# Kernel tuning notes

Hardware: AMD Instinct MI355X
Metric: run time of the kernel (lower is better)

## Reference

```python
import jax, jax.numpy as jnp
import numpy as np

N_NODES = 50000
N_EDGES = 800000
HEADS = 4
IN_CH = 128
HID_CH = 32   # per-head, conv1
OUT_CH = 32   # per-head, conv2
N_GRAPHS = 64
NEG_SLOPE = 0.2
BN_EPS = 1e-5


def gat_conv(x, src, dst, n_nodes, W, att_src, att_dst, bias):
    """PyG-style GATConv (concat heads). x:[N,Fin], W:[Fin,H*C], att_*:[H,C], bias:[H*C]."""
    H, C = att_src.shape
    h = (x @ W).reshape(n_nodes, H, C)                      # [N,H,C]
    a_src = jnp.einsum('nhc,hc->nh', h, att_src)            # [N,H]
    a_dst = jnp.einsum('nhc,hc->nh', h, att_dst)            # [N,H]
    e = jax.nn.leaky_relu(a_src[src] + a_dst[dst], NEG_SLOPE)  # [E,H]
    # segment softmax over incoming edges of each destination node
    e_max = jax.ops.segment_max(e, dst, num_segments=n_nodes)  # [N,H]
    alpha = jnp.exp(e - e_max[dst])                         # [E,H]
    denom = jax.ops.segment_sum(alpha, dst, num_segments=n_nodes)  # [N,H]
    alpha = alpha / denom[dst]
    msg = alpha[:, :, None] * h[src]                        # [E,H,C]
    out = jax.ops.segment_sum(msg, dst, num_segments=n_nodes)  # [N,H,C]
    return out.reshape(n_nodes, H * C) + bias


def setup_inputs() -> dict:
    key = jax.random.key(0)
    ks = jax.random.split(key, 12)
    d1 = HID_CH * HEADS  # 128
    d2 = OUT_CH * HEADS  # 128
    s_in = 1.0 / np.sqrt(IN_CH)
    s_h = 1.0 / np.sqrt(d1)
    return {
        'x': jax.random.normal(ks[0], (N_NODES, IN_CH), jnp.float32),
        'edge_index': jax.random.randint(ks[1], (2, N_EDGES), 0, N_NODES, jnp.int32),
        'batch': jnp.sort(jax.random.randint(ks[2], (N_NODES,), 0, N_GRAPHS, jnp.int32)),
        'W1': jax.random.normal(ks[3], (IN_CH, d1), jnp.float32) * s_in,
        'att_src1': jax.random.normal(ks[4], (HEADS, HID_CH), jnp.float32) * s_h,
        'att_dst1': jax.random.normal(ks[5], (HEADS, HID_CH), jnp.float32) * s_h,
        'bias1': jnp.zeros((d1,), jnp.float32),
        'gamma1': jnp.ones((d1,), jnp.float32),
        'beta1': jnp.zeros((d1,), jnp.float32),
        'W2': jax.random.normal(ks[6], (d1, d2), jnp.float32) * s_h,
        'att_src2': jax.random.normal(ks[7], (HEADS, OUT_CH), jnp.float32) * s_h,
        'att_dst2': jax.random.normal(ks[8], (HEADS, OUT_CH), jnp.float32) * s_h,
        'bias2': jnp.zeros((d2,), jnp.float32),
    }


def reference(x, edge_index, batch, W1, att_src1, att_dst1, bias1,
              gamma1, beta1, W2, att_src2, att_dst2, bias2):
    n = x.shape[0]
    loops = jnp.arange(n, dtype=edge_index.dtype)
    src = jnp.concatenate([edge_index[0], loops])  # add self-loops (PyG default)
    dst = jnp.concatenate([edge_index[1], loops])

    h = gat_conv(x, src, dst, n, W1, att_src1, att_dst1, bias1)
    # BatchNorm1d (batch statistics, biased variance), then ELU; dropout is inference no-op
    mu = h.mean(axis=0)
    var = h.var(axis=0)
    h = (h - mu) * jax.lax.rsqrt(var + BN_EPS) * gamma1 + beta1
    h = jax.nn.elu(h)

    h2 = gat_conv(h, src, dst, n, W2, att_src2, att_dst2, bias2)  # [N, OUT_CH*HEADS]

    # global mean pool over graphs
    ones = jnp.ones((n,), h2.dtype)
    counts = jax.ops.segment_sum(ones, batch, num_segments=N_GRAPHS)
    pooled = jax.ops.segment_sum(h2, batch, num_segments=N_GRAPHS)
    graph_rep = pooled / jnp.maximum(counts, 1.0)[:, None]
    return (h2, graph_rep)
```

## Files before the change

### kernel.cpp

```cpp
#include <hip/hip_runtime.h>

#define NN 50000
#define NE 800000
#define ET 850000
#define NG 64
#define D  128
#define NB 196
#define CAP 5120
#define CHUNK 8192

typedef unsigned short u16;
typedef unsigned int   u32;
typedef short bf16x8 __attribute__((ext_vector_type(8)));
typedef float f32x4  __attribute__((ext_vector_type(4)));

__device__ __forceinline__ u16 f2b(float f){
  u32 u = __float_as_uint(f);
  u32 r = (u + 0x7fffu + ((u >> 16) & 1u)) >> 16;
  return (u16)r;
}
__device__ __forceinline__ u32 pack2(float a, float b){
  return (u32)f2b(a) | ((u32)f2b(b) << 16);
}
__device__ __forceinline__ float lo16f(u32 u){ return __uint_as_float(u << 16); }
__device__ __forceinline__ float hi16f(u32 u){ return __uint_as_float(u & 0xffff0000u); }

__global__ void k_init(int* gCur, float* bsum, float* bsq, float* pooled){
  int i = blockIdx.x*256 + threadIdx.x;
  if (i < 256) gCur[i] = 0;
  if (i < 128){ bsum[i] = 0.f; bsq[i] = 0.f; }
  if (i < NG*D) pooled[i] = 0.f;
}

__global__ __launch_bounds__(256) void k_bucket(const int* __restrict__ srcE, const int* __restrict__ dstE,
                                                int* __restrict__ gCur, int* __restrict__ temp){
  __shared__ int hist[256], hbase[256], hpos[256], gbase[256];
  __shared__ int sorted[CHUNK];
  int tid = threadIdx.x;
  int e0 = blockIdx.x * CHUNK;
  int e1 = e0 + CHUNK; if (e1 > NE) e1 = NE;
  int cnt = e1 - e0;
  hist[tid] = 0;
  __syncthreads();
  for (int i = e0 + tid; i < e1; i += 256)
    atomicAdd(&hist[(u32)dstE[i] >> 8], 1);
  __syncthreads();
  int v = hist[tid];
  hbase[tid] = v;
  __syncthreads();
  for (int off = 1; off < 256; off <<= 1){
    int t = (tid >= off) ? hbase[tid-off] : 0;
    __syncthreads();
    hbase[tid] += t;
    __syncthreads();
  }
  int excl = hbase[tid] - v;
  __syncthreads();
  hbase[tid] = excl;
  hpos[tid]  = excl;
  __syncthreads();
  for (int i = e0 + tid; i < e1; i += 256){
    int d = dstE[i], sr = srcE[i];
    int idx = atomicAdd(&hpos[(u32)d >> 8], 1);
    sorted[idx] = (d << 16) | sr;
  }
  __syncthreads();
  if (tid < NB && hist[tid] > 0)
    gbase[tid] = atomicAdd(&gCur[tid], hist[tid]);
  __syncthreads();
  for (int i = tid; i < cnt; i += 256){
    int vv = sorted[i];
    int b = (u32)vv >> 24;
    int pos = gbase[b] + (i - hbase[b]);
    if (pos < CAP) temp[b*CAP + pos] = vv;
  }
}

__global__ void k_bstart(const int* __restrict__ gCur, int* __restrict__ bstart, int* __restrict__ offs){
  __shared__ int s[256];
  int tid = threadIdx.x;
  int nodes = (tid < NB) ? ((tid == NB-1) ? (NN - (NB-1)*256) : 256) : 0;
  int v = (tid < NB) ? gCur[tid] + nodes : 0;
  s[tid] = v;
  __syncthreads();
  for (int off = 1; off < 256; off <<= 1){
    int t = (tid >= off) ? s[tid-off] : 0;
    __syncthreads();
    s[tid] += t;
    __syncthreads();
  }
  if (tid < NB) bstart[tid] = s[tid] - v;
  if (tid == 0) offs[NN] = ET;
}

__global__ __launch_bounds__(256) void k_place(const int* __restrict__ temp, const int* __restrict__ gCur,
                                               const int* __restrict__ bstart, int* __restrict__ offs,
                                               int* __restrict__ srcs){
  __shared__ int cnt256[256], pfx[256], pos[256];
  int b = blockIdx.x, tid = threadIdx.x;
  int n0 = b << 8;
  int nNodes = NN - n0; if (nNodes > 256) nNodes = 256;
  int count = gCur[b];
  const int* tb = temp + b*CAP;
  cnt256[tid] = 0;
  __syncthreads();
  for (int i = tid; i < count; i += 256)
    atomicAdd(&cnt256[((u32)tb[i] >> 16) & 255], 1);
  __syncthreads();
  int own = cnt256[tid] + (tid < nNodes ? 1 : 0);
  pfx[tid] = own;
  __syncthreads();
  for (int off = 1; off < 256; off <<= 1){
    int t = (tid >= off) ? pfx[tid-off] : 0;
    __syncthreads();
    pfx[tid] += t;
    __syncthreads();
  }
  int excl = pfx[tid] - own;
  __syncthreads();
  pos[tid] = excl + 1;
  __syncthreads();
  int base = bstart[b];
  if (tid < nNodes){
    offs[n0 + tid] = base + excl;
    srcs[base + excl] = n0 + tid;
  }
  for (int i = tid; i < count; i += 256){
    int vv = tb[i];
    int d = ((u32)vv >> 16) & 255;
    int k = atomicAdd(&pos[d], 1);
    srcs[base + k] = vv & 0xFFFF;
  }
}

template<int FUSE_BN>
__global__ __launch_bounds__(512) void k_gemm(const float* __restrict__ X, const float* __restrict__ W,
                                              u16* __restrict__ Ybf,
                                              const float* __restrict__ att_s, const float* __restrict__ att_d,
                                              float* __restrict__ asrc, float* __restrict__ adst,
                                              const float* __restrict__ bsc, const float* __restrict__ bsh,
                                              int nrows){
  __shared__ u16 Xs[128*132];
  __shared__ u16 WT[128*132];
  int tid = threadIdx.x;
  int row0 = blockIdx.x * 128;
  #pragma unroll
  for (int t = 0; t < 8; t++){
    int i = tid + t*512;
    int r = i >> 5, k4 = i & 31;
    int gr = row0 + r;
    float4 v = (gr < nrows) ? ((const float4*)(X + (size_t)gr*D))[k4]
                            : make_float4(0.f,0.f,0.f,0.f);
    if (FUSE_BN){
      float4 sc = ((const float4*)bsc)[k4];
      float4 sh = ((const float4*)bsh)[k4];
      v.x = fmaf(v.x, sc.x, sh.x); v.y = fmaf(v.y, sc.y, sh.y);
      v.z = fmaf(v.z, sc.z, sh.z); v.w = fmaf(v.w, sc.w, sh.w);
      v.x = v.x > 0.f ? v.x : expm1f(v.x);
      v.y = v.y > 0.f ? v.y : expm1f(v.y);
      v.z = v.z > 0.f ? v.z : expm1f(v.z);
      v.w = v.w > 0.f ? v.w : expm1f(v.w);
    }
    *(uint2*)&Xs[r*132 + k4*4] = make_uint2(pack2(v.x, v.y), pack2(v.z, v.w));
  }
  {
    int c = tid & 127, kp = tid >> 7;
    #pragma unroll
    for (int t = 0; t < 16; t++){
      int kk = kp + t*4;
      float w0 = W[(size_t)(2*kk)*D + c];
      float w1 = W[(size_t)(2*kk+1)*D + c];
      *(u32*)&WT[c*132 + 2*kk] = pack2(w0, w1);
    }
  }
  __syncthreads();
  int w = tid >> 6, l = tid & 63;
  int l15 = l & 15, lq = l >> 4;
  int cw = w*16;
  bf16x8 bfr[4];
  #pragma unroll
  for (int ks = 0; ks < 4; ks++)
    bfr[ks] = *(const bf16x8*)&WT[(cw + l15)*132 + ks*32 + lq*8];
  f32x4 acc[8];
  #pragma unroll
  for (int m = 0; m < 8; m++) acc[m] = (f32x4){0.f,0.f,0.f,0.f};
  #pragma unroll
  for (int m = 0; m < 8; m++){
    #pragma unroll
    for (int ks = 0; ks < 4; ks++){
      bf16x8 af = *(const bf16x8*)&Xs[(m*16 + l15)*132 + ks*32 + lq*8];
      acc[m] = __builtin_amdgcn_mfma_f32_16x16x32_bf16(af, bfr[ks], acc[m], 0, 0, 0);
    }
  }
  __syncthreads();
  float* sDotS = (float*)Xs;
  float* sDotD = sDotS + 1024;
  {
    float as_c = att_s[cw + l15];
    float ad_c = att_d[cw + l15];
    #pragma unroll
    for (int m = 0; m < 8; m++){
      #pragma unroll
      for (int i = 0; i < 4; i++){
        float ps = acc[m][i] * as_c;
        float pd = acc[m][i] * ad_c;
        #pragma unroll
        for (int msk = 1; msk <= 8; msk <<= 1){
          ps += __shfl_xor(ps, msk);
          pd += __shfl_xor(pd, msk);
        }
        if (l15 == 0){
          int r = m*16 + lq*4 + i;
          sDotS[w*128 + r] = ps;
          sDotD[w*128 + r] = pd;
        }
      }
    }
  }
  #pragma unroll
  for (int m = 0; m < 8; m++){
    #pragma unroll
    for (int i = 0; i < 4; i++){
      float v = acc[m][i];
      float nb = __shfl_xor(v, 1);
      if (!(l & 1)){
        int gr = row0 + m*16 + lq*4 + i;
        if (gr < nrows)
          *(u32*)&Ybf[(size_t)gr*D + cw + l15] = pack2(v, nb);
      }
    }
  }
  __syncthreads();
  {
    int r = tid >> 2, h = tid & 3;
    int gr = row0 + r;
    if (gr < nrows){
      asrc[gr*4 + h] = sDotS[(2*h)*128 + r] + sDotS[(2*h+1)*128 + r];
      adst[gr*4 + h] = sDotD[(2*h)*128 + r] + sDotD[(2*h+1)*128 + r];
    }
  }
}

__global__ __launch_bounds__(256) void k_edge(
                       const u16* __restrict__ hb, const float* __restrict__ asrc,
                       const float* __restrict__ adst, const int* __restrict__ offs,
                       const int* __restrict__ srcs, const float* __restrict__ bias,
                       float* __restrict__ out){
  __shared__ uint2 sPk[4][4][17];
  int w = threadIdx.x >> 6;
  int lane = threadIdx.x & 63;
  int n = blockIdx.x*4 + w;
  int off0 = offs[n];
  int deg  = offs[n+1] - off0;
  int hd = lane >> 4, j16 = lane & 15;
  float adh = adst[n*4 + hd];
  int half = lane >> 5, q = lane & 31;
  int hg = q >> 3;
  int qb = q*8;
  float denp = 0.f;
  float acc0=0.f, acc1=0.f, acc2=0.f, acc3=0.f;
  const char* hbase = (const char*)hb;
  const int* sp = srcs + off0;
  int sj = (j16 < deg) ? sp[j16] : 0;
  float av = asrc[sj*4 + hd];
  for (int base = 0; base < deg; base += 16){
    int lim = deg - base; if (lim > 16) lim = 16;
    int nbase = base + 16;
    bool hasn = (nbase < deg);
    int sjn = 0;
    if (hasn){
      int idx = nbase + j16;
      sjn = (idx < deg) ? sp[idx] : 0;
    }
    float al;
    if (j16 < lim){
      float e = av + adh;
      e = e > 0.f ? e : 0.2f*e;
      al = __expf(e);
    } else al = 0.f;
    denp += al;
    sPk[w][hd][j16] = make_uint2((u32)sj << 8, __float_as_uint(al));
    float avn = hasn ? asrc[sjn*4 + hd] : 0.f;
    if (lim == 16){
      uint2 p0 = sPk[w][hg][half],      p1 = sPk[w][hg][2+half];
      uint2 p2 = sPk[w][hg][4+half],    p3 = sPk[w][hg][6+half];
      uint2 p4 = sPk[w][hg][8+half],    p5 = sPk[w][hg][10+half];
      uint2 p6 = sPk[w][hg][12+half],   p7 = sPk[w][hg][14+half];
      uint2 v0 = *(const uint2*)(hbase + p0.x + qb);
      uint2 v1 = *(const uint2*)(hbase + p1.x + qb);
      uint2 v2 = *(const uint2*)(hbase + p2.x + qb);
      uint2 v3 = *(const uint2*)(hbase + p3.x + qb);
      uint2 v4 = *(const uint2*)(hbase + p4.x + qb);
      uint2 v5 = *(const uint2*)(hbase + p5.x + qb);
      uint2 v6 = *(const uint2*)(hbase + p6.x + qb);
      uint2 v7 = *(const uint2*)(hbase + p7.x + qb);
      float a0 = __uint_as_float(p0.y), a1 = __uint_as_float(p1.y);
      float a2 = __uint_as_float(p2.y), a3 = __uint_as_float(p3.y);
      float a4 = __uint_as_float(p4.y), a5 = __uint_as_float(p5.y);
      float a6 = __uint_as_float(p6.y), a7 = __uint_as_float(p7.y);
      acc0 = fmaf(a0, lo16f(v0.x), acc0); acc1 = fmaf(a0, hi16f(v0.x), acc1);
      acc2 = fmaf(a0, lo16f(v0.y), acc2); acc3 = fmaf(a0, hi16f(v0.y), acc3);
      acc0 = fmaf(a1, lo16f(v1.x), acc0); acc1 = fmaf(a1, hi16f(v1.x), acc1);
      acc2 = fmaf(a1, lo16f(v1.y), acc2); acc3 = fmaf(a1, hi16f(v1.y), acc3);
      acc0 = fmaf(a2, lo16f(v2.x), acc0); acc1 = fmaf(a2, hi16f(v2.x), acc1);
      acc2 = fmaf(a2, lo16f(v2.y), acc2); acc3 = fmaf(a2, hi16f(v2.y), acc3);
      acc0 = fmaf(a3, lo16f(v3.x), acc0); acc1 = fmaf(a3, hi16f(v3.x), acc1);
      acc2 = fmaf(a3, lo16f(v3.y), acc2); acc3 = fmaf(a3, hi16f(v3.y), acc3);
      acc0 = fmaf(a4, lo16f(v4.x), acc0); acc1 = fmaf(a4, hi16f(v4.x), acc1);
      acc2 = fmaf(a4, lo16f(v4.y), acc2); acc3 = fmaf(a4, hi16f(v4.y), acc3);
      acc0 = fmaf(a5, lo16f(v5.x), acc0); acc1 = fmaf(a5, hi16f(v5.x), acc1);
      acc2 = fmaf(a5, lo16f(v5.y), acc2); acc3 = fmaf(a5, hi16f(v5.y), acc3);
      acc0 = fmaf(a6, lo16f(v6.x), acc0); acc1 = fmaf(a6, hi16f(v6.x), acc1);
      acc2 = fmaf(a6, lo16f(v6.y), acc2); acc3 = fmaf(a6, hi16f(v6.y), acc3);
      acc0 = fmaf(a7, lo16f(v7.x), acc0); acc1 = fmaf(a7, hi16f(v7.x), acc1);
      acc2 = fmaf(a7, lo16f(v7.y), acc2); acc3 = fmaf(a7, hi16f(v7.y), acc3);
    } else {
      for (int j = 0; j < lim; j += 8){
        uint2 pA = sPk[w][hg][j+half],   pB = sPk[w][hg][j+2+half];
        uint2 pC = sPk[w][hg][j+4+half], pD = sPk[w][hg][j+6+half];
        uint2 vA = *(const uint2*)(hbase + pA.x + qb);
        uint2 vB = *(const uint2*)(hbase + pB.x + qb);
        uint2 vC = *(const uint2*)(hbase + pC.x + qb);
        uint2 vD = *(const uint2*)(hbase + pD.x + qb);
        float aA = __uint_as_float(pA.y), aB = __uint_as_float(pB.y);
        float aC = __uint_as_float(pC.y), aD = __uint_as_float(pD.y);
        acc0 = fmaf(aA, lo16f(vA.x), acc0); acc1 = fmaf(aA, hi16f(vA.x), acc1);
        acc2 = fmaf(aA, lo16f(vA.y), acc2); acc3 = fmaf(aA, hi16f(vA.y), acc3);
        acc0 = fmaf(aB, lo16f(vB.x), acc0); acc1 = fmaf(aB, hi16f(vB.x), acc1);
        acc2 = fmaf(aB, lo16f(vB.y), acc2); acc3 = fmaf(aB, hi16f(vB.y), acc3);
        acc0 = fmaf(aC, lo16f(vC.x), acc0); acc1 = fmaf(aC, hi16f(vC.x), acc1);
        acc2 = fmaf(aC, lo16f(vC.y), acc2); acc3 = fmaf(aC, hi16f(vC.y), acc3);
        acc0 = fmaf(aD, lo16f(vD.x), acc0); acc1 = fmaf(aD, hi16f(vD.x), acc1);
        acc2 = fmaf(aD, lo16f(vD.y), acc2); acc3 = fmaf(aD, hi16f(vD.y), acc3);
      }
    }
    sj = sjn; av = avn;
  }
  denp += __shfl_xor(denp, 1);
  denp += __shfl_xor(denp, 2);
  denp += __shfl_xor(denp, 4);
  denp += __shfl_xor(denp, 8);
  acc0 += __shfl_xor(acc0, 32);
  acc1 += __shfl_xor(acc1, 32);
  acc2 += __shfl_xor(acc2, 32);
  acc3 += __shfl_xor(acc3, 32);
  float inv = 1.f / __shfl(denp, hg*16);
  if (half == 0){
    int cb = q*4;
    float4 o;
    o.x = acc0*inv + bias[cb];
    o.y = acc1*inv + bias[cb+1];
    o.z = acc2*inv + bias[cb+2];
    o.w = acc3*inv + bias[cb+3];
    ((float4*)(out + (size_t)n*D))[q] = o;
  }
}

__global__ __launch_bounds__(256) void k_bnstat(const float* __restrict__ B,
                                                float* __restrict__ bsum, float* __restrict__ bsq){
  __shared__ float sS[256], sQ[256];
  int tid = threadIdx.x;
  int c = tid & 127;
  int rr = tid >> 7;
  int r0 = blockIdx.x * 64;
  int r1 = r0 + 64; if (r1 > NN) r1 = NN;
  float s = 0.f, qv = 0.f;
  for (int r = r0 + rr; r < r1; r += 2){
    float v = B[(size_t)r*D + c];
    s += v; qv += v*v;
  }
  sS[tid] = s; sQ[tid] = qv;
  __syncthreads();
  if (tid < 128){
    atomicAdd(&bsum[c], sS[tid] + sS[tid+128]);
    atomicAdd(&bsq[c],  sQ[tid] + sQ[tid+128]);
  }
}

__global__ void k_bnfin(const float* __restrict__ bsum, const float* __restrict__ bsq,
                        const float* __restrict__ gamma, const float* __restrict__ beta,
                        float* __restrict__ scale, float* __restrict__ shift){
  int c = threadIdx.x;
  float mu  = bsum[c] * (1.f/NN);
  float var = bsq[c] * (1.f/NN) - mu*mu;
  float sc  = gamma[c] * rsqrtf(var + 1e-5f);
  scale[c] = sc;
  shift[c] = beta[c] - mu*sc;
}

#define POOL_ROWS 50
__global__ void k_poolA(const float* __restrict__ h2, const int* __restrict__ batch,
                        float* __restrict__ pooled){
  int c = threadIdx.x & 127;
  int half = threadIdx.x >> 7;
  int r0 = blockIdx.x * POOL_ROWS;
  int r1 = r0 + POOL_ROWS; if (r1 > NN) r1 = NN;
  float s = 0.f; int g = -1;
  for (int r = r0 + half; r < r1; r += 2){
    int bg = batch[r];
    if (bg != g){
      if (g >= 0) atomicAdd(&pooled[g*D + c], s);
      g = bg; s = 0.f;
    }
    s += h2[(size_t)r*D + c];
  }
  if (g >= 0) atomicAdd(&pooled[g*D + c], s);
}

__global__ void k_poolB(const float* __restrict__ pooled, const int* __restrict__ batch,
                        float* __restrict__ out){
  int g = blockIdx.x;
  int c = threadIdx.x;
  int lo = 0, hi = NN;
  while (lo < hi){ int mid = (lo+hi) >> 1; if (batch[mid] < g) lo = mid+1; else hi = mid; }
  int a = lo, b = NN;
  while (a < b){ int mid = (a+b) >> 1; if (batch[mid] < g+1) a = mid+1; else b = mid; }
  int cntg = a - lo;
  out[g*D + c] = pooled[g*D + c] / (float)(cntg > 1 ? cntg : 1);
}

extern "C" void kernel_launch(void* const* d_in, const int* in_sizes, int n_in,
                              void* d_out, int out_size, void* d_ws, size_t ws_size,
                              hipStream_t stream){
  (void)in_sizes; (void)n_in; (void)out_size; (void)ws_size;
  const float* x   = (const float*)d_in[0];
  const int* ei    = (const int*)d_in[1];
  const int* batch = (const int*)d_in[2];
  const float* W1  = (const float*)d_in[3];
  const float* as1 = (const float*)d_in[4];
  const float* ad1 = (const float*)d_in[5];
  const float* b1  = (const float*)d_in[6];
  const float* g1  = (const float*)d_in[7];
  const float* be1 = (const float*)d_in[8];
  const float* W2  = (const float*)d_in[9];
  const float* as2 = (const float*)d_in[10];
  const float* ad2 = (const float*)d_in[11];
  const float* b2  = (const float*)d_in[12];
  float* outp = (float*)d_out;

  float* B    = (float*)d_ws;
  float* asr  = B + 6400000;
  float* ads  = asr + 200000;
  float* bsum = ads + 200000;
  float* bsq  = bsum + 128;
  float* bsc  = bsq + 128;
  float* bsh  = bsc + 128;
  float* pooled = bsh + 128;
  int* gCur   = (int*)(pooled + NG*D);
  int* bstart = gCur + 256;
  int* offs   = bstart + 256;
  int* srcs   = offs + (NN+1);
  int* temp   = srcs + ET;
  u16* hb     = (u16*)(temp + NB*CAP);

  const int* srcE = ei;
  const int* dstE = ei + NE;

  k_init<<<32, 256, 0, stream>>>(gCur, bsum, bsq, pooled);
  k_gemm<0><<<391, 512, 0, stream>>>(x, W1, hb, as1, ad1, asr, ads, nullptr, nullptr, NN);
  k_bucket<<<(NE + CHUNK - 1)/CHUNK, 256, 0, stream>>>(srcE, dstE, gCur, temp);
  k_bstart<<<1, 256, 0, stream>>>(gCur, bstart, offs);
  k_place<<<NB, 256, 0, stream>>>(temp, gCur, bstart, offs, srcs);
  k_edge<<<NN/4, 256, 0, stream>>>(hb, asr, ads, offs, srcs, b1, B);
  k_bnstat<<<782, 256, 0, stream>>>(B, bsum, bsq);
  k_bnfin<<<1, 128, 0, stream>>>(bsum, bsq, g1, be1, bsc, bsh);
  k_gemm<1><<<391, 512, 0, stream>>>(B, W2, hb, as2, ad2, asr, ads, bsc, bsh, NN);
  k_edge<<<NN/4, 256, 0, stream>>>(hb, asr, ads, offs, srcs, b2, outp);
  k_poolA<<<(NN + POOL_ROWS - 1)/POOL_ROWS, 256, 0, stream>>>(outp, batch, pooled);
  k_poolB<<<NG, 128, 0, stream>>>(pooled, batch, outp + 6400000);
}
```

Measured before the change: 233.9 us.

## Use head-major feature layout and one-head-per-block edge aggregation

Node features and source attention scores are now stored head-major, so each block in the edge kernel handles one head for four nodes. That gives 4x more blocks, and each gather is a contiguous 64-byte head slice processed 8 edges at a time per wave. The weight matrices are transposed and converted to bf16 once by a new prep kernel, so every GEMM block no longer re-transposes W. The LDS row pitch is also changed to 136. The risk is that offsets, srcs and adst are read four times, each gather is smaller, and there are two extra launches.

```diff
diff --git a/kernel.cpp b/kernel.cpp
--- a/kernel.cpp
+++ b/kernel.cpp
@@ -30,6 +30,13 @@
   if (i < 256) gCur[i] = 0;
   if (i < 128){ bsum[i] = 0.f; bsq[i] = 0.f; }
   if (i < NG*D) pooled[i] = 0.f;
+}
+
+__global__ void k_prepw(const float* __restrict__ W, u16* __restrict__ WTb){
+  for (int i = blockIdx.x*256 + threadIdx.x; i < D*D; i += gridDim.x*256){
+    int c = i >> 7, k = i & 127;
+    WTb[i] = f2b(W[(size_t)k*D + c]);
+  }
 }
 
 __global__ __launch_bounds__(256) void k_bucket(const int* __restrict__ srcE, const int* __restrict__ dstE,
@@ -134,14 +141,14 @@
 }
 
 template<int FUSE_BN>
-__global__ __launch_bounds__(512) void k_gemm(const float* __restrict__ X, const float* __restrict__ W,
-                                              u16* __restrict__ Ybf,
+__global__ __launch_bounds__(512) void k_gemm(const float* __restrict__ X, const u16* __restrict__ WTb,
+                                              u16* __restrict__ hbT,
                                               const float* __restrict__ att_s, const float* __restrict__ att_d,
-                                              float* __restrict__ asrc, float* __restrict__ adst,
+                                              float* __restrict__ asrcT, float* __restrict__ adst,
                                               const float* __restrict__ bsc, const float* __restrict__ bsh,
                                               int nrows){
-  __shared__ u16 Xs[128*132];
-  __shared__ u16 WT[128*132];
+  __shared__ u16 Xs[128*136];
+  __shared__ u16 WT[128*136];
   int tid = threadIdx.x;
   int row0 = blockIdx.x * 128;
   #pragma unroll
@@ -161,17 +168,14 @@
       v.z = v.z > 0.f ? v.z : expm1f(v.z);
       v.w = v.w > 0.f ? v.w : expm1f(v.w);
     }
-    *(uint2*)&Xs[r*132 + k4*4] = make_uint2(pack2(v.x, v.y), pack2(v.z, v.w));
-  }
-  {
-    int c = tid & 127, kp = tid >> 7;
-    #pragma unroll
-    for (int t = 0; t < 16; t++){
-      int kk = kp + t*4;
-      float w0 = W[(size_t)(2*kk)*D + c];
-      float w1 = W[(size_t)(2*kk+1)*D + c];
-      *(u32*)&WT[c*132 + 2*kk] = pack2(w0, w1);
-    }
+    *(uint2*)&Xs[r*136 + k4*4] = make_uint2(pack2(v.x, v.y), pack2(v.z, v.w));
+  }
+  #pragma unroll
+  for (int t = 0; t < 4; t++){
+    int i = tid + t*512;
+    int c = i >> 4, k16 = i & 15;
+    uint4 vv = ((const uint4*)WTb)[i];
+    *(uint4*)&WT[c*136 + k16*8] = vv;
   }
   __syncthreads();
   int w = tid >> 6, l = tid & 63;
@@ -180,7 +184,7 @@
   bf16x8 bfr[4];
   #pragma unroll
   for (int ks = 0; ks < 4; ks++)
-    bfr[ks] = *(const bf16x8*)&WT[(cw + l15)*132 + ks*32 + lq*8];
+    bfr[ks] = *(const bf16x8*)&WT[(cw + l15)*136 + ks*32 + lq*8];
   f32x4 acc[8];
   #pragma unroll
   for (int m = 0; m < 8; m++) acc[m] = (f32x4){0.f,0.f,0.f,0.f};
@@ -188,7 +192,7 @@
   for (int m = 0; m < 8; m++){
     #pragma unroll
     for (int ks = 0; ks < 4; ks++){
-      bf16x8 af = *(const bf16x8*)&Xs[(m*16 + l15)*132 + ks*32 + lq*8];
+      bf16x8 af = *(const bf16x8*)&Xs[(m*16 + l15)*136 + ks*32 + lq*8];
       acc[m] = __builtin_amdgcn_mfma_f32_16x16x32_bf16(af, bfr[ks], acc[m], 0, 0, 0);
     }
   }
@@ -225,8 +229,11 @@
       float nb = __shfl_xor(v, 1);
       if (!(l & 1)){
         int gr = row0 + m*16 + lq*4 + i;
-        if (gr < nrows)
-          *(u32*)&Ybf[(size_t)gr*D + cw + l15] = pack2(v, nb);
+        if (gr < nrows){
+          int col = cw + l15;
+          int head = col >> 5, c32 = col & 31;
+          *(u32*)&hbT[((size_t)head*NN + gr)*32 + c32] = pack2(v, nb);
+        }
       }
     }
   }
@@ -235,124 +242,82 @@
     int r = tid >> 2, h = tid & 3;
     int gr = row0 + r;
     if (gr < nrows){
-      asrc[gr*4 + h] = sDotS[(2*h)*128 + r] + sDotS[(2*h+1)*128 + r];
+      asrcT[(size_t)h*NN + gr] = sDotS[(2*h)*128 + r] + sDotS[(2*h+1)*128 + r];
       adst[gr*4 + h] = sDotD[(2*h)*128 + r] + sDotD[(2*h+1)*128 + r];
     }
   }
 }
 
 __global__ __launch_bounds__(256) void k_edge(
-                       const u16* __restrict__ hb, const float* __restrict__ asrc,
+                       const u16* __restrict__ hbT, const float* __restrict__ asrcT,
                        const float* __restrict__ adst, const int* __restrict__ offs,
                        const int* __restrict__ srcs, const float* __restrict__ bias,
                        float* __restrict__ out){
-  __shared__ uint2 sPk[4][4][17];
+  __shared__ uint2 sAl[4][64];
   int w = threadIdx.x >> 6;
   int lane = threadIdx.x & 63;
-  int n = blockIdx.x*4 + w;
+  int h = blockIdx.x & 3;
+  int n = (blockIdx.x >> 2)*4 + w;
   int off0 = offs[n];
   int deg  = offs[n+1] - off0;
-  int hd = lane >> 4, j16 = lane & 15;
-  float adh = adst[n*4 + hd];
-  int half = lane >> 5, q = lane & 31;
-  int hg = q >> 3;
-  int qb = q*8;
+  float adh = adst[n*4 + h];
+  const float* asp = asrcT + (size_t)h*NN;
+  const char* hbase = (const char*)(hbT + (size_t)h*NN*32);
+  const int* sp = srcs + off0;
+  int g8 = lane & 7;
+  int eg = lane >> 3;
   float denp = 0.f;
   float acc0=0.f, acc1=0.f, acc2=0.f, acc3=0.f;
-  const char* hbase = (const char*)hb;
-  const int* sp = srcs + off0;
-  int sj = (j16 < deg) ? sp[j16] : 0;
-  float av = asrc[sj*4 + hd];
-  for (int base = 0; base < deg; base += 16){
-    int lim = deg - base; if (lim > 16) lim = 16;
-    int nbase = base + 16;
-    bool hasn = (nbase < deg);
-    int sjn = 0;
-    if (hasn){
-      int idx = nbase + j16;
-      sjn = (idx < deg) ? sp[idx] : 0;
-    }
-    float al;
-    if (j16 < lim){
-      float e = av + adh;
+  for (int base = 0; base < deg; base += 64){
+    int lim = deg - base; if (lim > 64) lim = 64;
+    int sj = 0; float al = 0.f;
+    if (lane < lim){
+      sj = sp[base + lane];
+      float e = asp[sj] + adh;
       e = e > 0.f ? e : 0.2f*e;
       al = __expf(e);
-    } else al = 0.f;
+    }
     denp += al;
-    sPk[w][hd][j16] = make_uint2((u32)sj << 8, __float_as_uint(al));
-    float avn = hasn ? asrc[sjn*4 + hd] : 0.f;
-    if (lim == 16){
-      uint2 p0 = sPk[w][hg][half],      p1 = sPk[w][hg][2+half];
-      uint2 p2 = sPk[w][hg][4+half],    p3 = sPk[w][hg][6+half];
-      uint2 p4 = sPk[w][hg][8+half],    p5 = sPk[w][hg][10+half];
-      uint2 p6 = sPk[w][hg][12+half],   p7 = sPk[w][hg][14+half];
-      uint2 v0 = *(const uint2*)(hbase + p0.x + qb);
-      uint2 v1 = *(const uint2*)(hbase + p1.x + qb);
-      uint2 v2 = *(const uint2*)(hbase + p2.x + qb);
-      uint2 v3 = *(const uint2*)(hbase + p3.x + qb);
-      uint2 v4 = *(const uint2*)(hbase + p4.x + qb);
-      uint2 v5 = *(const uint2*)(hbase + p5.x + qb);
-      uint2 v6 = *(const uint2*)(hbase + p6.x + qb);
-      uint2 v7 = *(const uint2*)(hbase + p7.x + qb);
-      float a0 = __uint_as_float(p0.y), a1 = __uint_as_float(p1.y);
-      float a2 = __uint_as_float(p2.y), a3 = __uint_as_float(p3.y);
-      float a4 = __uint_as_float(p4.y), a5 = __uint_as_float(p5.y);
-      float a6 = __uint_as_float(p6.y), a7 = __uint_as_float(p7.y);
-      acc0 = fmaf(a0, lo16f(v0.x), acc0); acc1 = fmaf(a0, hi16f(v0.x), acc1);
-      acc2 = fmaf(a0, lo16f(v0.y), acc2); acc3 = fmaf(a0, hi16f(v0.y), acc3);
-      acc0 = fmaf(a1, lo16f(v1.x), acc0); acc1 = fmaf(a1, hi16f(v1.x), acc1);
-      acc2 = fmaf(a1, lo16f(v1.y), acc2); acc3 = fmaf(a1, hi16f(v1.y), acc3);
-      acc0 = fmaf(a2, lo16f(v2.x), acc0); acc1 = fmaf(a2, hi16f(v2.x), acc1);
-      acc2 = fmaf(a2, lo16f(v2.y), acc2); acc3 = fmaf(a2, hi16f(v2.y), acc3);
-      acc0 = fmaf(a3, lo16f(v3.x), acc0); acc1 = fmaf(a3, hi16f(v3.x), acc1);
-      acc2 = fmaf(a3, lo16f(v3.y), acc2); acc3 = fmaf(a3, hi16f(v3.y), acc3);
-      acc0 = fmaf(a4, lo16f(v4.x), acc0); acc1 = fmaf(a4, hi16f(v4.x), acc1);
-      acc2 = fmaf(a4, lo16f(v4.y), acc2); acc3 = fmaf(a4, hi16f(v4.y), acc3);
-      acc0 = fmaf(a5, lo16f(v5.x), acc0); acc1 = fmaf(a5, hi16f(v5.x), acc1);
-      acc2 = fmaf(a5, lo16f(v5.y), acc2); acc3 = fmaf(a5, hi16f(v5.y), acc3);
-      acc0 = fmaf(a6, lo16f(v6.x), acc0); acc1 = fmaf(a6, hi16f(v6.x), acc1);
-      acc2 = fmaf(a6, lo16f(v6.y), acc2); acc3 = fmaf(a6, hi16f(v6.y), acc3);
-      acc0 = fmaf(a7, lo16f(v7.x), acc0); acc1 = fmaf(a7, hi16f(v7.x), acc1);
-      acc2 = fmaf(a7, lo16f(v7.y), acc2); acc3 = fmaf(a7, hi16f(v7.y), acc3);
-    } else {
-      for (int j = 0; j < lim; j += 8){
-        uint2 pA = sPk[w][hg][j+half],   pB = sPk[w][hg][j+2+half];
-        uint2 pC = sPk[w][hg][j+4+half], pD = sPk[w][hg][j+6+half];
-        uint2 vA = *(const uint2*)(hbase + pA.x + qb);
-        uint2 vB = *(const uint2*)(hbase + pB.x + qb);
-        uint2 vC = *(const uint2*)(hbase + pC.x + qb);
-        uint2 vD = *(const uint2*)(hbase + pD.x + qb);
-        float aA = __uint_as_float(pA.y), aB = __uint_as_float(pB.y);
-        float aC = __uint_as_float(pC.y), aD = __uint_as_float(pD.y);
-        acc0 = fmaf(aA, lo16f(vA.x), acc0); acc1 = fmaf(aA, hi16f(vA.x), acc1);
-        acc2 = fmaf(aA, lo16f(vA.y), acc2); acc3 = fmaf(aA, hi16f(vA.y), acc3);
-        acc0 = fmaf(aB, lo16f(vB.x), acc0); acc1 = fmaf(aB, hi16f(vB.x), acc1);
-        acc2 = fmaf(aB, lo16f(vB.y), acc2); acc3 = fmaf(aB, hi16f(vB.y), acc3);
-        acc0 = fmaf(aC, lo16f(vC.x), acc0); acc1 = fmaf(aC, hi16f(vC.x), acc1);
-        acc2 = fmaf(aC, lo16f(vC.y), acc2); acc3 = fmaf(aC, hi16f(vC.y), acc3);
-        acc0 = fmaf(aD, lo16f(vD.x), acc0); acc1 = fmaf(aD, hi16f(vD.x), acc1);
-        acc2 = fmaf(aD, lo16f(vD.y), acc2); acc3 = fmaf(aD, hi16f(vD.y), acc3);
-      }
-    }
-    sj = sjn; av = avn;
-  }
-  denp += __shfl_xor(denp, 1);
-  denp += __shfl_xor(denp, 2);
-  denp += __shfl_xor(denp, 4);
-  denp += __shfl_xor(denp, 8);
-  acc0 += __shfl_xor(acc0, 32);
-  acc1 += __shfl_xor(acc1, 32);
-  acc2 += __shfl_xor(acc2, 32);
-  acc3 += __shfl_xor(acc3, 32);
-  float inv = 1.f / __shfl(denp, hg*16);
-  if (half == 0){
-    int cb = q*4;
+    sAl[w][lane] = make_uint2((u32)sj*64, __float_as_uint(al));
+    int rounds = (lim + 7) >> 3;
+    int r = 0;
+    for (; r + 2 <= rounds; r += 2){
+      uint2 pkA = sAl[w][r*8 + eg];
+      uint2 pkB = sAl[w][r*8 + 8 + eg];
+      uint2 vA = *(const uint2*)(hbase + pkA.x + g8*8);
+      uint2 vB = *(const uint2*)(hbase + pkB.x + g8*8);
+      float aA = __uint_as_float(pkA.y), aB = __uint_as_float(pkB.y);
+      acc0 = fmaf(aA, lo16f(vA.x), acc0); acc1 = fmaf(aA, hi16f(vA.x), acc1);
+      acc2 = fmaf(aA, lo16f(vA.y), acc2); acc3 = fmaf(aA, hi16f(vA.y), acc3);
+      acc0 = fmaf(aB, lo16f(vB.x), acc0); acc1 = fmaf(aB, hi16f(vB.x), acc1);
+      acc2 = fmaf(aB, lo16f(vB.y), acc2); acc3 = fmaf(aB, hi16f(vB.y), acc3);
+    }
+    if (r < rounds){
+      uint2 pk = sAl[w][r*8 + eg];
+      uint2 v = *(const uint2*)(hbase + pk.x + g8*8);
+      float a = __uint_as_float(pk.y);
+      acc0 = fmaf(a, lo16f(v.x), acc0); acc1 = fmaf(a, hi16f(v.x), acc1);
+      acc2 = fmaf(a, lo16f(v.y), acc2); acc3 = fmaf(a, hi16f(v.y), acc3);
+    }
+  }
+  acc0 += __shfl_xor(acc0, 8);  acc1 += __shfl_xor(acc1, 8);
+  acc2 += __shfl_xor(acc2, 8);  acc3 += __shfl_xor(acc3, 8);
+  acc0 += __shfl_xor(acc0, 16); acc1 += __shfl_xor(acc1, 16);
+  acc2 += __shfl_xor(acc2, 16); acc3 += __shfl_xor(acc3, 16);
+  acc0 += __shfl_xor(acc0, 32); acc1 += __shfl_xor(acc1, 32);
+  acc2 += __shfl_xor(acc2, 32); acc3 += __shfl_xor(acc3, 32);
+  denp += __shfl_xor(denp, 1);  denp += __shfl_xor(denp, 2);
+  denp += __shfl_xor(denp, 4);  denp += __shfl_xor(denp, 8);
+  denp += __shfl_xor(denp, 16); denp += __shfl_xor(denp, 32);
+  float inv = 1.f / denp;
+  if (lane < 8){
+    int cb = h*32 + lane*4;
     float4 o;
     o.x = acc0*inv + bias[cb];
     o.y = acc1*inv + bias[cb+1];
     o.z = acc2*inv + bias[cb+2];
     o.w = acc3*inv + bias[cb+3];
-    ((float4*)(out + (size_t)n*D))[q] = o;
+    *(float4*)(out + (size_t)n*D + cb) = o;
   }
 }
 
@@ -439,8 +404,8 @@
   float* outp = (float*)d_out;
 
   float* B    = (float*)d_ws;
-  float* asr  = B + 6400000;
-  float* ads  = asr + 200000;
+  float* asrcT= B + 6400000;
+  float* ads  = asrcT + 200000;
   float* bsum = ads + 200000;
   float* bsq  = bsum + 128;
   float* bsc  = bsq + 128;
@@ -451,21 +416,25 @@
   int* offs   = bstart + 256;
   int* srcs   = offs + (NN+1);
   int* temp   = srcs + ET;
-  u16* hb     = (u16*)(temp + NB*CAP);
+  u16* hbT    = (u16*)(temp + NB*CAP);
+  u16* WTb1   = hbT + 6400000;
+  u16* WTb2   = WTb1 + D*D;
 
   const int* srcE = ei;
   const int* dstE = ei + NE;
 
   k_init<<<32, 256, 0, stream>>>(gCur, bsum, bsq, pooled);
-  k_gemm<0><<<391, 512, 0, stream>>>(x, W1, hb, as1, ad1, asr, ads, nullptr, nullptr, NN);
+  k_prepw<<<32, 256, 0, stream>>>(W1, WTb1);
+  k_prepw<<<32, 256, 0, stream>>>(W2, WTb2);
+  k_gemm<0><<<391, 512, 0, stream>>>(x, WTb1, hbT, as1, ad1, asrcT, ads, nullptr, nullptr, NN);
   k_bucket<<<(NE + CHUNK - 1)/CHUNK, 256, 0, stream>>>(srcE, dstE, gCur, temp);
   k_bstart<<<1, 256, 0, stream>>>(gCur, bstart, offs);
   k_place<<<NB, 256, 0, stream>>>(temp, gCur, bstart, offs, srcs);
-  k_edge<<<NN/4, 256, 0, stream>>>(hb, asr, ads, offs, srcs, b1, B);
+  k_edge<<<NN, 256, 0, stream>>>(hbT, asrcT, ads, offs, srcs, b1, B);
   k_bnstat<<<782, 256, 0, stream>>>(B, bsum, bsq);
   k_bnfin<<<1, 128, 0, stream>>>(bsum, bsq, g1, be1, bsc, bsh);
-  k_gemm<1><<<391, 512, 0, stream>>>(B, W2, hb, as2, ad2, asr, ads, bsc, bsh, NN);
-  k_edge<<<NN/4, 256, 0, stream>>>(hb, asr, ads, offs, srcs, b2, outp);
+  k_gemm<1><<<391, 512, 0, stream>>>(B, WTb2, hbT, as2, ad2, asrcT, ads, bsc, bsh, NN);
+  k_edge<<<NN, 256, 0, stream>>>(hbT, asrcT, ads, offs, srcs, b2, outp);
   k_poolA<<<(NN + POOL_ROWS - 1)/POOL_ROWS, 256, 0, stream>>>(outp, batch, pooled);
   k_poolB<<<NG, 128, 0, stream>>>(pooled, batch, outp + 6400000);
 }
```

Result: slower. 292.6 us (+25.1%).
